# Kernel tuning notes

Hardware: AMD Instinct MI355X
Metric: run time of the kernel (lower is better)

## Reference

```python
import jax, jax.numpy as jnp
import numpy as np

B = 16384
IN_DIM = 28 * 28
HID = 768
NUM_EXPERTS = 8
NUM_CLASSES = 10
H_PHASOR = 32          # phasor bank harmonics -> 2*H features
DELTA0 = 7.0
DECAY = 0.7            # spiking attention leak
THETA = 1.0
K_WINNERS = 5
TOP_K_ROUTE = 2
TRAITS = (0.6, 0.6, 0.5, 0.5, 0.4)


def setup_inputs() -> dict:
    key = jax.random.key(0)
    ks = jax.random.split(key, 16)
    s = 0.02
    return {
        "x": jax.random.normal(ks[0], (B, 28, 28), jnp.float32),
        "W_in": jax.random.normal(ks[1], (IN_DIM, HID), jnp.float32) * s,
        "b_in": jnp.zeros((HID,), jnp.float32),
        "W_ph": jax.random.normal(ks[2], (2 * H_PHASOR, HID), jnp.float32) * s,
        "b_ph": jnp.zeros((HID,), jnp.float32),
        "W_gate": jax.random.normal(ks[3], (HID, NUM_EXPERTS), jnp.float32) * s,
        "b_gate": jnp.zeros((NUM_EXPERTS,), jnp.float32),
        "W_exp": jax.random.normal(ks[4], (NUM_EXPERTS, HID, HID), jnp.float32) * s,
        "b_exp": jnp.zeros((NUM_EXPERTS, HID), jnp.float32),
        "W_th": jax.random.normal(ks[5], (HID, NUM_EXPERTS), jnp.float32) * s,
        "b_th": jnp.zeros((NUM_EXPERTS,), jnp.float32),
        "W_pm": jax.random.normal(ks[6], (5, NUM_EXPERTS), jnp.float32) * s,
        "b_pm": jnp.zeros((NUM_EXPERTS,), jnp.float32),
        "W_out": jax.random.normal(ks[7], (HID, NUM_CLASSES), jnp.float32) * s,
        "b_out": jnp.zeros((NUM_CLASSES,), jnp.float32),
    }


def reference(x, W_in, b_in, W_ph, b_ph, W_gate, b_gate, W_exp, b_exp,
              W_th, b_th, W_pm, b_pm, W_out, b_out):
    Bn = x.shape[0]
    x_flat = x.reshape((Bn, -1))
    proj = x_flat @ W_in + b_in                                  # [B, HID]

    # Phasor bank on per-sample mean activation: sin/cos at H harmonics
    x_mean = jnp.mean(proj, axis=-1)                             # [B]
    freqs = DELTA0 * jnp.arange(1, H_PHASOR + 1, dtype=proj.dtype)
    phase = x_mean[:, None] * freqs[None, :]                     # [B, H]
    feats = jnp.concatenate([jnp.sin(phase), jnp.cos(phase)], -1)  # [B, 2H]
    enhanced = proj + feats @ W_ph + b_ph                        # [B, HID]

    # Top-K index selection feeding gather/scatter spiking attention
    V = enhanced.shape[-1]
    K = min(32, V)
    topk_idx = jax.lax.top_k(enhanced, K)[1].astype(jnp.int32)   # [B, K]
    w = DECAY ** jnp.arange(K, dtype=enhanced.dtype)             # decaying drive

    def gains_fn(idx):
        v = jnp.zeros((V,), enhanced.dtype).at[idx].add(w)       # scatter-add
        vals, widx = jax.lax.top_k(v, K_WINNERS)                 # k-WTA
        return jnp.ones((V,), enhanced.dtype).at[widx].add(vals / THETA)

    gains = jax.vmap(gains_fn)(topk_idx)                         # [B, V]
    attended = enhanced * gains

    # Personality bias + thalamic bias (thalamic_scale = 1.0)
    traits = jnp.asarray(TRAITS, dtype=enhanced.dtype)
    pbias = traits @ W_pm + b_pm                                 # [E]
    thal = jnp.mean(attended, axis=0) @ W_th + b_th              # [E]

    # MoE retrieval core: gate -> top-k softmax route -> combine experts
    gate_logits = attended @ W_gate + b_gate + pbias[None] + thal[None]  # [B, E]
    gvals, gidx = jax.lax.top_k(gate_logits, TOP_K_ROUTE)        # [B, k]
    gw = jax.nn.softmax(gvals, axis=-1)                          # [B, k]
    exp_out = jnp.einsum('bh,ehd->bed', attended, W_exp) + b_exp[None]   # [B, E, HID]
    sel = jnp.take_along_axis(exp_out, gidx[:, :, None], axis=1)  # [B, k, HID]
    context = jnp.sum(gw[:, :, None] * sel, axis=1)              # [B, HID]

    return context @ W_out + b_out                               # [B, classes]
```

## Files before the change

kernel.cpp:

```cpp
#include <hip/hip_runtime.h>
#include <hip/hip_bf16.h>
#include <cstddef>

#define BATCH 16384
#define IND   784
#define HID   768
#define NEXP  8
#define KT13  13

typedef short bf16x8 __attribute__((ext_vector_type(8)));
typedef float f32x4  __attribute__((ext_vector_type(4)));
typedef unsigned short ushort_t;

#define GLD16(g, l)                                                            \
  __builtin_amdgcn_global_load_lds(                                            \
      (const __attribute__((address_space(1))) unsigned int*)(g),              \
      (__attribute__((address_space(3))) unsigned int*)(l), 16, 0, 0)

__global__ __launch_bounds__(256) void k_wtrans(const float* __restrict__ Wexp,
                                                __hip_bfloat16* __restrict__ Wt)
{
  __shared__ float tile[32][33];
  const int e = blockIdx.z;
  const int h0 = blockIdx.x * 32, d0 = blockIdx.y * 32;
  const int tx = threadIdx.x & 31, ty = threadIdx.x >> 5;
  const float* src = Wexp + ((size_t)e * HID + h0) * HID + d0;
  #pragma unroll
  for (int i = 0; i < 4; i++)
    tile[ty + 8 * i][tx] = src[(size_t)(ty + 8 * i) * HID + tx];
  __syncthreads();
  __hip_bfloat16* dst = Wt + ((size_t)e * HID + d0) * HID + h0;
  #pragma unroll
  for (int i = 0; i < 4; i++)
    dst[(size_t)(ty + 8 * i) * HID + tx] = __float2bfloat16(tile[tx][ty + 8 * i]);
}

__device__ inline ushort_t bf16_rne(float f) {
  union { float f; unsigned u; } v; v.f = f;
  unsigned r = v.u + 0x7fffu + ((v.u >> 16) & 1u);
  return (ushort_t)(r >> 16);
}
__device__ inline float bf16_to_f(ushort_t h) {
  union { unsigned u; float f; } v; v.u = ((unsigned)h) << 16;
  return v.f;
}

__global__ __launch_bounds__(256) void k_packA(const float* __restrict__ x,
                                               ushort_t* __restrict__ Ahi,
                                               ushort_t* __restrict__ Alo)
{
  const int kt = blockIdx.x, mt = blockIdx.y;
  const size_t tbase = ((size_t)mt * KT13 + kt) * 8192;
  const int kb = kt * 64;
  #pragma unroll
  for (int i = 0; i < 4; i++) {
    int id = i * 256 + threadIdx.x;
    int r = id >> 3, c = id & 7;
    int row = mt * 128 + r;
    int k0 = kb + c * 8;
    float v[8];
    if (k0 + 8 <= IND) {
      const float4* p = reinterpret_cast<const float4*>(x + (size_t)row * IND + k0);
      float4 a = p[0], b = p[1];
      v[0] = a.x; v[1] = a.y; v[2] = a.z; v[3] = a.w;
      v[4] = b.x; v[5] = b.y; v[6] = b.z; v[7] = b.w;
    } else {
      #pragma unroll
      for (int j = 0; j < 8; j++) v[j] = (k0 + j < IND) ? x[(size_t)row * IND + k0 + j] : 0.f;
    }
    ushort_t hi[8], lo[8];
    #pragma unroll
    for (int j = 0; j < 8; j++) {
      hi[j] = bf16_rne(v[j]);
      lo[j] = bf16_rne(v[j] - bf16_to_f(hi[j]));
    }
    size_t dst = tbase + (size_t)r * 64 + ((c ^ (r & 7)) * 8);
    *reinterpret_cast<uint4*>(Ahi + dst) = *reinterpret_cast<uint4*>(hi);
    *reinterpret_cast<uint4*>(Alo + dst) = *reinterpret_cast<uint4*>(lo);
  }
}

__global__ __launch_bounds__(256) void k_packB(const float* __restrict__ W,
                                               ushort_t* __restrict__ Bhi,
                                               ushort_t* __restrict__ Blo)
{
  const int kt = blockIdx.x, nt = blockIdx.y;
  const size_t tbase = ((size_t)nt * KT13 + kt) * 8192;
  const int kb = kt * 64;
  #pragma unroll
  for (int i = 0; i < 4; i++) {
    int id = i * 256 + threadIdx.x;
    int r = id >> 3, c = id & 7;
    int n = nt * 128 + r;
    int k0 = kb + c * 8;
    float v[8];
    #pragma unroll
    for (int j = 0; j < 8; j++)
      v[j] = (k0 + j < IND) ? W[(size_t)(k0 + j) * HID + n] : 0.f;
    ushort_t hi[8], lo[8];
    #pragma unroll
    for (int j = 0; j < 8; j++) {
      hi[j] = bf16_rne(v[j]);
      lo[j] = bf16_rne(v[j] - bf16_to_f(hi[j]));
    }
    size_t dst = tbase + (size_t)r * 64 + ((c ^ (r & 7)) * 8);
    *reinterpret_cast<uint4*>(Bhi + dst) = *reinterpret_cast<uint4*>(hi);
    *reinterpret_cast<uint4*>(Blo + dst) = *reinterpret_cast<uint4*>(lo);
  }
}

__global__ __launch_bounds__(256, 2) void k_proj2(const ushort_t* __restrict__ Ahi,
                                                  const ushort_t* __restrict__ Alo,
                                                  const ushort_t* __restrict__ Bhi,
                                                  const ushort_t* __restrict__ Blo,
                                                  const float* __restrict__ bias,
                                                  float* __restrict__ out,
                                                  float* __restrict__ pm)
{
  __shared__ __align__(16) ushort_t lds[4 * 8192];
  const int bid = blockIdx.x;
  const int sid = (bid & 7) * 96 + (bid >> 3);
  const int mt = sid / 6, nt = sid - 6 * mt;
  const int tid = threadIdx.x, lane = tid & 63, w = tid >> 6;
  const int m0 = (w >> 1) * 64, n0 = (w & 1) * 64;
  const int l15 = lane & 15, g = lane >> 4;

  f32x4 acc[4][4];
  #pragma unroll
  for (int i = 0; i < 4; i++)
    #pragma unroll
    for (int j = 0; j < 4; j++) acc[i][j] = (f32x4){0.f, 0.f, 0.f, 0.f};

  const size_t abase = (size_t)mt * KT13 * 8192;
  const size_t bbase = (size_t)nt * KT13 * 8192;

  for (int kt = 0; kt < KT13; kt++) {
    __syncthreads();
    const ushort_t* srcs[4] = { Ahi + abase + (size_t)kt * 8192,
                                Alo + abase + (size_t)kt * 8192,
                                Bhi + bbase + (size_t)kt * 8192,
                                Blo + bbase + (size_t)kt * 8192 };
    #pragma unroll
    for (int buf = 0; buf < 4; buf++) {
      #pragma unroll
      for (int i = 0; i < 4; i++) {
        int off = w * 2048 + i * 512 + lane * 8;
        GLD16(srcs[buf] + off, &lds[buf * 8192 + w * 2048 + i * 512]);
      }
    }
    asm volatile("s_waitcnt vmcnt(0)");
    __syncthreads();
    #pragma unroll
    for (int ks = 0; ks < 2; ks++) {
      bf16x8 ah[4], al[4], bh[4], bl[4];
      #pragma unroll
      for (int i = 0; i < 4; i++) {
        int ca = ((4 * ks + g) ^ (l15 & 7)) * 8;
        int ra = m0 + 16 * i + l15;
        ah[i] = *reinterpret_cast<const bf16x8*>(&lds[0 * 8192 + ra * 64 + ca]);
        al[i] = *reinterpret_cast<const bf16x8*>(&lds[1 * 8192 + ra * 64 + ca]);
        int rb = n0 + 16 * i + l15;
        bh[i] = *reinterpret_cast<const bf16x8*>(&lds[2 * 8192 + rb * 64 + ca]);
        bl[i] = *reinterpret_cast<const bf16x8*>(&lds[3 * 8192 + rb * 64 + ca]);
      }
      #pragma unroll
      for (int i = 0; i < 4; i++)
        #pragma unroll
        for (int j = 0; j < 4; j++) {
          acc[i][j] = __builtin_amdgcn_mfma_f32_16x16x32_bf16(ah[i], bh[j], acc[i][j], 0, 0, 0);
          acc[i][j] = __builtin_amdgcn_mfma_f32_16x16x32_bf16(ah[i], bl[j], acc[i][j], 0, 0, 0);
          acc[i][j] = __builtin_amdgcn_mfma_f32_16x16x32_bf16(al[i], bh[j], acc[i][j], 0, 0, 0);
        }
    }
  }
  float bl[4];
  #pragma unroll
  for (int j = 0; j < 4; j++) bl[j] = bias[nt * 128 + n0 + 16 * j + l15];
  #pragma unroll
  for (int i = 0; i < 4; i++) {
    #pragma unroll
    for (int q = 0; q < 4; q++) {
      int m = mt * 128 + m0 + 16 * i + g * 4 + q;
      #pragma unroll
      for (int j = 0; j < 4; j++) {
        int n = nt * 128 + n0 + 16 * j + l15;
        out[(size_t)m * HID + n] = acc[i][j][q] + bl[j];
      }
    }
  }
  const float blsum = bl[0] + bl[1] + bl[2] + bl[3];
  const size_t pslot = (size_t)(nt * 2 + (w & 1)) * BATCH;
  #pragma unroll
  for (int i = 0; i < 4; i++) {
    #pragma unroll
    for (int q = 0; q < 4; q++) {
      float s = acc[i][0][q] + acc[i][1][q] + acc[i][2][q] + acc[i][3][q] + blsum;
      s += __shfl_xor(s, 1); s += __shfl_xor(s, 2);
      s += __shfl_xor(s, 4); s += __shfl_xor(s, 8);
      if (l15 == 0)
        pm[pslot + mt * 128 + m0 + 16 * i + g * 4 + q] = s;
    }
  }
}

__global__ __launch_bounds__(256) void k_phasor(const float* __restrict__ pm,
                                                const float* __restrict__ Wph,
                                                const float* __restrict__ bph,
                                                float* __restrict__ enh)
{
  __shared__ float Fs[64][132];
  __shared__ float Ws[64][128];
  __shared__ float mlds[128];
  const int t  = threadIdx.x;
  const int bm = blockIdx.y * 128, bn = blockIdx.x * 128;
  if (t < 128) {
    float s = 0.f;
    #pragma unroll
    for (int k = 0; k < 12; k++) s += pm[(size_t)k * BATCH + bm + t];
    mlds[t] = s * (1.0f / 768.0f);
  }
  __syncthreads();
  {
    const int r = t >> 1;
    const float mn = mlds[r];
    if ((t & 1) == 0) {
      #pragma unroll
      for (int j = 0; j < 32; j++) Fs[j][r] = sinf(mn * (7.0f * (j + 1)));
    } else {
      #pragma unroll
      for (int j = 0; j < 32; j++) Fs[32 + j][r] = cosf(mn * (7.0f * (j + 1)));
    }
  }
  #pragma unroll
  for (int i = 0; i < 8; i++) {
    int f4 = i * 256 + t;
    int k = f4 >> 5, n4 = (f4 & 31) * 4;
    *reinterpret_cast<float4*>(&Ws[k][n4]) =
        *reinterpret_cast<const float4*>(Wph + (size_t)k * HID + bn + n4);
  }
  __syncthreads();

  const int m0 = (t >> 4) * 8, n0 = (t & 15) * 8;
  float acc[8][8];
  #pragma unroll
  for (int i = 0; i < 8; i++)
    #pragma unroll
    for (int j = 0; j < 8; j++) acc[i][j] = 0.f;
  #pragma unroll 4
  for (int k = 0; k < 64; k++) {
    float a[8], b[8];
    *reinterpret_cast<float4*>(&a[0]) = *reinterpret_cast<const float4*>(&Fs[k][m0]);
    *reinterpret_cast<float4*>(&a[4]) = *reinterpret_cast<const float4*>(&Fs[k][m0 + 4]);
    *reinterpret_cast<float4*>(&b[0]) = *reinterpret_cast<const float4*>(&Ws[k][n0]);
    *reinterpret_cast<float4*>(&b[4]) = *reinterpret_cast<const float4*>(&Ws[k][n0 + 4]);
    #pragma unroll
    for (int i = 0; i < 8; i++)
      #pragma unroll
      for (int j = 0; j < 8; j++) acc[i][j] = fmaf(a[i], b[j], acc[i][j]);
  }
  float bl[8];
  #pragma unroll
  for (int j = 0; j < 8; j++) bl[j] = bph[bn + n0 + j];
  #pragma unroll
  for (int i = 0; i < 8; i++) {
    float* rowp = enh + (size_t)(bm + m0 + i) * HID + bn + n0;
    float4 p0 = *reinterpret_cast<float4*>(rowp);
    float4 p1 = *reinterpret_cast<float4*>(rowp + 4);
    p0.x += acc[i][0] + bl[0]; p0.y += acc[i][1] + bl[1];
    p0.z += acc[i][2] + bl[2]; p0.w += acc[i][3] + bl[3];
    p1.x += acc[i][4] + bl[4]; p1.y += acc[i][5] + bl[5];
    p1.z += acc[i][6] + bl[6]; p1.w += acc[i][7] + bl[7];
    *reinterpret_cast<float4*>(rowp)     = p0;
    *reinterpret_cast<float4*>(rowp + 4) = p1;
  }
}

__global__ __launch_bounds__(256) void k_attend(const float* __restrict__ enh,
                                                const float* __restrict__ Wg,
                                                __hip_bfloat16* __restrict__ attb,
                                                float* __restrict__ glog,
                                                float* __restrict__ partials)
{
  __shared__ float WgT[8][768];
  __shared__ float cs[4][768];
  const int t = threadIdx.x, lane = t & 63, w = t >> 6;
  for (int i = t; i < 768 * 8; i += 256) { int c = i >> 3, e = i & 7; WgT[e][c] = Wg[i]; }
  for (int i = t; i < 4 * 768; i += 256) cs[i / 768][i % 768] = 0.f;
  __syncthreads();

  for (int rr = 0; rr < 8; ++rr) {
    const int row = blockIdx.x * 32 + rr * 4 + w;
    const float* er = enh + (size_t)row * HID;
    float o[12], s[12];
    #pragma unroll
    for (int j = 0; j < 12; j++) { o[j] = er[lane + 64 * j]; s[j] = o[j]; }

    int wc[5];
    #pragma unroll
    for (int k = 0; k < 5; k++) {
      float v = -3.4e38f; int c = 0x7fffffff;
      #pragma unroll
      for (int j = 0; j < 12; j++)
        if (s[j] > v) { v = s[j]; c = lane + 64 * j; }
      #pragma unroll
      for (int off = 32; off; off >>= 1) {
        float ov = __shfl_xor(v, off); int oc = __shfl_xor(c, off);
        if (ov > v || (ov == v && oc < c)) { v = ov; c = oc; }
      }
      wc[k] = c;
      if (lane == (c & 63)) {
        #pragma unroll
        for (int j = 0; j < 12; j++) if (j == (c >> 6)) s[j] = -3.4e38f;
      }
    }

    float a[12];
    #pragma unroll
    for (int j = 0; j < 12; j++) a[j] = o[j];
    float wv = 1.0f;
    #pragma unroll
    for (int k = 0; k < 5; k++) {
      int c = wc[k];
      if (lane == (c & 63)) {
        #pragma unroll
        for (int j = 0; j < 12; j++) if (j == (c >> 6)) a[j] = o[j] * (1.0f + wv);
      }
      wv *= 0.7f;
    }
    #pragma unroll
    for (int j = 0; j < 12; j++)
      attb[(size_t)row * HID + lane + 64 * j] = __float2bfloat16(a[j]);
    #pragma unroll
    for (int j = 0; j < 12; j++) cs[w][lane + 64 * j] += a[j];

    float p[8];
    #pragma unroll
    for (int e = 0; e < 8; e++) p[e] = 0.f;
    #pragma unroll
    for (int j = 0; j < 12; j++) {
      int c = lane + 64 * j;
      #pragma unroll
      for (int e = 0; e < 8; e++) p[e] = fmaf(a[j], WgT[e][c], p[e]);
    }
    #pragma unroll
    for (int e = 0; e < 8; e++) {
      #pragma unroll
      for (int off = 32; off; off >>= 1) p[e] += __shfl_xor(p[e], off);
    }
    if (lane == 0) {
      #pragma unroll
      for (int e = 0; e < 8; e++) glog[(size_t)row * 8 + e] = p[e];
    }
  }
  __syncthreads();
  for (int i = t; i < 768; i += 256)
    partials[(size_t)blockIdx.x * 768 + i] = cs[0][i] + cs[1][i] + cs[2][i] + cs[3][i];
}

__global__ void k_thal(const float* __restrict__ partials,
                       const float* __restrict__ Wth, const float* __restrict__ bth,
                       const float* __restrict__ Wpm, const float* __restrict__ bpm,
                       const float* __restrict__ bgate, float* __restrict__ add8)
{
  __shared__ float cm[768];
  __shared__ float th[8];
  const int t = threadIdx.x;
  float s = 0.f;
  #pragma unroll 8
  for (int b = 0; b < 512; b++) s += partials[(size_t)b * 768 + t];
  cm[t] = s * (1.0f / 16384.0f);
  __syncthreads();
  if (t < 256) {
    int e = t >> 5, l = t & 31;
    float ps = 0.f;
    for (int c = l; c < 768; c += 32) ps = fmaf(cm[c], Wth[(size_t)c * 8 + e], ps);
    #pragma unroll
    for (int off = 16; off; off >>= 1) ps += __shfl_xor(ps, off);
    if (l == 0) th[e] = ps + bth[e];
  }
  __syncthreads();
  if (t < 8) {
    const float TR[5] = {0.6f, 0.6f, 0.5f, 0.5f, 0.4f};
    float pb = bpm[t];
    #pragma unroll
    for (int i = 0; i < 5; i++) pb = fmaf(TR[i], Wpm[i * 8 + t], pb);
    add8[t] = th[t] + pb + bgate[t];
  }
}

__global__ __launch_bounds__(256) void k_route(const float* __restrict__ glog,
                                               const float* __restrict__ add8,
                                               float* __restrict__ rw,
                                               unsigned char* __restrict__ re,
                                               int* __restrict__ counts)
{
  __shared__ float a8[8];
  __shared__ int lc[8];
  const int t = threadIdx.x;
  if (t < 8) { a8[t] = add8[t]; lc[t] = 0; }
  __syncthreads();
  const int row = blockIdx.x * 256 + t;
  const float4* gp = reinterpret_cast<const float4*>(glog + (size_t)row * 8);
  float4 g0 = gp[0], g1 = gp[1];
  float l[8] = { g0.x + a8[0], g0.y + a8[1], g0.z + a8[2], g0.w + a8[3],
                 g1.x + a8[4], g1.y + a8[5], g1.z + a8[6], g1.w + a8[7] };
  float v0 = l[0], v1 = -3.4e38f; int i0 = 0, i1 = 0;
  #pragma unroll
  for (int e = 1; e < 8; e++) {
    if (l[e] > v0)      { v1 = v0; i1 = i0; v0 = l[e]; i0 = e; }
    else if (l[e] > v1) { v1 = l[e]; i1 = e; }
  }
  float ex = expf(v1 - v0);
  float inv = 1.0f / (1.0f + ex);
  rw[row * 2] = inv; rw[row * 2 + 1] = ex * inv;
  re[row * 2] = (unsigned char)i0; re[row * 2 + 1] = (unsigned char)i1;
  atomicAdd(&lc[i0], 1); atomicAdd(&lc[i1], 1);
  __syncthreads();
  if (t < 8) atomicAdd(&counts[t], lc[t]);
}

__global__ void k_prefix(const int* __restrict__ counts, int* __restrict__ meta)
{
  if (threadIdx.x == 0) {
    int o = 0, tt = 0;
    for (int e = 0; e < 8; e++) {
      meta[e] = o; meta[9 + e] = tt; meta[19 + e] = o;
      o += counts[e]; tt += (counts[e] + 127) >> 7;
    }
    meta[8] = o; meta[17] = tt; meta[18] = tt;
  }
}

__global__ __launch_bounds__(256) void k_scatter(const unsigned char* __restrict__ re,
                                                 int* __restrict__ meta,
                                                 int* __restrict__ perm,
                                                 int* __restrict__ inv)
{
  __shared__ int lc[8], base[8];
  const int t = threadIdx.x;
  if (t < 8) lc[t] = 0;
  __syncthreads();
  const int row = blockIdx.x * 256 + t;
  const int e0 = re[row * 2], e1 = re[row * 2 + 1];
  const int p0 = atomicAdd(&lc[e0], 1);
  const int p1 = atomicAdd(&lc[e1], 1);
  __syncthreads();
  if (t < 8) base[t] = atomicAdd(&meta[19 + t], lc[t]);
  __syncthreads();
  const int s0 = base[e0] + p0;
  const int s1 = base[e1] + p1;
  perm[s0] = row * 2;     inv[row * 2]     = s0;
  perm[s1] = row * 2 + 1; inv[row * 2 + 1] = s1;
}

__global__ __launch_bounds__(256) void k_expert(const unsigned short* __restrict__ attb,
                                                const unsigned short* __restrict__ Wt,
                                                const float* __restrict__ bexp,
                                                const float* __restrict__ rw,
                                                const int* __restrict__ perm,
                                                const int* __restrict__ meta,
                                                ushort_t* __restrict__ ctxP)
{
  const int l = blockIdx.x;
  const int xcd = l & 7, idx = l >> 3;
  const int tb = xcd + 8 * (idx / 6);
  const int nb = (idx - 6 * (idx / 6)) * 128;
  if (tb >= meta[18]) return;
  __shared__ __align__(16) ushort_t sst[2][2][8192];
  __shared__ int rid[128];
  __shared__ float gws[128];
  __shared__ float bxs[128];

  const int* tst = meta + 9;
  int e = 0;
  #pragma unroll
  for (int i = 1; i < 8; i++) if (tb >= tst[i]) e = i;
  const int tix  = tb - tst[e];
  const int off  = meta[e];
  const int cnt  = meta[e + 1] - off;
  const int rbase = off + tix * 128;
  const int vcnt  = min(128, cnt - tix * 128);
  const int tid = threadIdx.x;

  if (tid < 128) {
    if (tid < vcnt) {
      int p = perm[rbase + tid];
      rid[tid] = p >> 1; gws[tid] = rw[p];
    } else {
      rid[tid] = 0; gws[tid] = 0.f;
    }
    bxs[tid] = bexp[(size_t)e * HID + nb + tid];
  }
  __syncthreads();

  const int lane = tid & 63, w = tid >> 6;
  const int m0 = (w >> 1) * 64, n0 = (w & 1) * 64;
  const int l15 = lane & 15, g = lane >> 4;
  const unsigned short* wbase = Wt + ((size_t)e * HID + nb) * HID;

#define ESTAGE(kb, b)                                                          \
  { _Pragma("unroll")                                                          \
    for (int i = 0; i < 4; i++) {                                              \
      int id_ = i * 256 + tid; int r_ = id_ >> 3, c_ = id_ & 7;                \
      int sc_ = (c_ ^ (r_ & 7)) * 8;                                           \
      GLD16(attb + (size_t)rid[r_] * HID + (kb) + sc_, &sst[b][0][(i * 256 + w * 64) * 8]); \
      GLD16(wbase + (size_t)r_ * HID + (kb) + sc_,     &sst[b][1][(i * 256 + w * 64) * 8]); \
    } }

  f32x4 acc[4][4];
  #pragma unroll
  for (int i = 0; i < 4; i++)
    #pragma unroll
    for (int j = 0; j < 4; j++) acc[i][j] = (f32x4){0.f, 0.f, 0.f, 0.f};

  ESTAGE(0, 0);
  for (int t = 0; t < 12; t++) {
    const int cb = t & 1;
    if (t < 11) {
      ESTAGE((t + 1) * 64, cb ^ 1);
      asm volatile("s_waitcnt vmcnt(8)" ::: "memory");
    } else {
      asm volatile("s_waitcnt vmcnt(0)" ::: "memory");
    }
    __builtin_amdgcn_s_barrier();
    const ushort_t* As = &sst[cb][0][0];
    const ushort_t* Bs = &sst[cb][1][0];
    #pragma unroll
    for (int ks = 0; ks < 2; ks++) {
      bf16x8 af[4], bfr[4];
      #pragma unroll
      for (int i = 0; i < 4; i++) {
        int ca = (((4 * ks + g) ^ (l15 & 7)) * 8);
        af[i]  = *reinterpret_cast<const bf16x8*>(As + (m0 + 16 * i + l15) * 64 + ca);
        bfr[i] = *reinterpret_cast<const bf16x8*>(Bs + (n0 + 16 * i + l15) * 64 + ca);
      }
      #pragma unroll
      for (int i = 0; i < 4; i++)
        #pragma unroll
        for (int j = 0; j < 4; j++)
          acc[i][j] = __builtin_amdgcn_mfma_f32_16x16x32_bf16(af[i], bfr[j], acc[i][j], 0, 0, 0);
    }
    __builtin_amdgcn_s_barrier();
  }
#undef ESTAGE

  unsigned short* Cs = &sst[0][0][0];
  __syncthreads();
  #pragma unroll
  for (int i = 0; i < 4; i++) {
    #pragma unroll
    for (int q = 0; q < 4; q++) {
      int m = m0 + 16 * i + g * 4 + q;
      float gwv = gws[m];
      #pragma unroll
      for (int j = 0; j < 4; j++) {
        int n = n0 + 16 * j + l15;
        Cs[m * 128 + n] = bf16_rne(gwv * (acc[i][j][q] + bxs[n]));
      }
    }
  }
  __syncthreads();
  #pragma unroll
  for (int c = 0; c < 8; c++) {
    int r = w * 32 + c * 4 + (lane >> 4);
    if (r < vcnt) {
      uint4 v = *reinterpret_cast<const uint4*>(Cs + r * 128 + l15 * 8);
      *reinterpret_cast<uint4*>(ctxP + (size_t)(rbase + r) * HID + nb + l15 * 8) = v;
    }
  }
}

__global__ __launch_bounds__(256) void k_out(const ushort_t* __restrict__ ctxP,
                                             const int* __restrict__ inv,
                                             const float* __restrict__ Wout,
                                             const float* __restrict__ bout,
                                             float* __restrict__ out)
{
  __shared__ float wT[10][768];
  const int t = threadIdx.x, lane = t & 63, w = t >> 6;
  for (int i = t; i < 7680; i += 256) { int cl = i / 768, d = i - cl * 768; wT[cl][d] = Wout[(size_t)d * 10 + cl]; }
  __syncthreads();
  for (int rr = 0; rr < 8; ++rr) {
    const int row = blockIdx.x * 32 + rr * 4 + w;
    const int s0 = inv[row * 2], s1 = inv[row * 2 + 1];
    const ushort_t* p0 = ctxP + (size_t)s0 * HID;
    const ushort_t* p1 = ctxP + (size_t)s1 * HID;
    float cd[12];
    #pragma unroll
    for (int j = 0; j < 12; j++)
      cd[j] = bf16_to_f(p0[lane + 64 * j]) + bf16_to_f(p1[lane + 64 * j]);
    float p[10];
    #pragma unroll
    for (int cl = 0; cl < 10; cl++) {
      float ps = 0.f;
      #pragma unroll
      for (int j = 0; j < 12; j++) ps = fmaf(cd[j], wT[cl][lane + 64 * j], ps);
      #pragma unroll
      for (int off = 32; off; off >>= 1) ps += __shfl_xor(ps, off);
      p[cl] = ps;
    }
    if (lane == 0) {
      #pragma unroll
      for (int cl = 0; cl < 10; cl++) out[(size_t)row * 10 + cl] = p[cl] + bout[cl];
    }
  }
}

extern "C" void kernel_launch(void* const* d_in, const int* in_sizes, int n_in,
                              void* d_out, int out_size, void* d_ws, size_t ws_size,
                              hipStream_t stream)
{
  const float* x     = (const float*)d_in[0];
  const float* W_in  = (const float*)d_in[1];
  const float* b_in  = (const float*)d_in[2];
  const float* W_ph  = (const float*)d_in[3];
  const float* b_ph  = (const float*)d_in[4];
  const float* W_g   = (const float*)d_in[5];
  const float* b_g   = (const float*)d_in[6];
  const float* W_exp = (const float*)d_in[7];
  const float* b_exp = (const float*)d_in[8];
  const float* W_th  = (const float*)d_in[9];
  const float* b_th  = (const float*)d_in[10];
  const float* W_pm  = (const float*)d_in[11];
  const float* b_pm  = (const float*)d_in[12];
  const float* W_out = (const float*)d_in[13];
  const float* b_out = (const float*)d_in[14];
  float* out = (float*)d_out;

  char* ws = (char*)d_ws;
  size_t off = 0;
  float* enh = (float*)(ws + off); off += (size_t)BATCH * HID * 4;
  char*  r1  = ws + off;           off += (size_t)2 * BATCH * KT13 * 64 * 2;
  ushort_t* Ahi = (ushort_t*)r1;
  ushort_t* Alo = Ahi + (size_t)BATCH * KT13 * 64;
  __hip_bfloat16* attb = (__hip_bfloat16*)r1;
  __hip_bfloat16* Wt   = (__hip_bfloat16*)(r1 + (size_t)BATCH * HID * 2);
  float* glog     = (float*)(ws + off); off += (size_t)BATCH * 8 * 4;
  float* partials = (float*)(ws + off); off += (size_t)512 * 768 * 4;
  float* pm       = (float*)(ws + off); off += (size_t)12 * BATCH * 4;
  float* add8     = (float*)(ws + off); off += 256;
  float* rw       = (float*)(ws + off); off += (size_t)BATCH * 2 * 4;
  unsigned char* re = (unsigned char*)(ws + off); off += (size_t)BATCH * 2;
  int* counts = (int*)(ws + off); off += 256;
  int* meta   = (int*)(ws + off); off += 256;
  int* perm   = (int*)(ws + off); off += (size_t)BATCH * 2 * 4;
  int* invp   = (int*)(ws + off); off += (size_t)BATCH * 2 * 4;
  ushort_t* Bhi = (ushort_t*)(ws + off); off += (size_t)KT13 * 64 * HID * 2;
  ushort_t* Blo = (ushort_t*)(ws + off); off += (size_t)KT13 * 64 * HID * 2;
  ushort_t* ctxP = (ushort_t*)enh;

  hipMemsetAsync(counts, 0, 32, stream);
  k_packB <<<dim3(13, 6),     256, 0, stream>>>(W_in, Bhi, Blo);
  k_packA <<<dim3(13, 128),   256, 0, stream>>>(x, Ahi, Alo);
  k_proj2 <<<768,             256, 0, stream>>>(Ahi, Alo, Bhi, Blo, b_in, enh, pm);
  k_wtrans<<<dim3(24, 24, 8), 256, 0, stream>>>(W_exp, Wt);
  k_phasor<<<dim3(6, 128),    256, 0, stream>>>(pm, W_ph, b_ph, enh);
  k_attend<<<512,             256, 0, stream>>>(enh, W_g, attb, glog, partials);
  k_thal  <<<1,               768, 0, stream>>>(partials, W_th, b_th, W_pm, b_pm, b_g, add8);
  k_route <<<64,              256, 0, stream>>>(glog, add8, rw, re, counts);
  k_prefix<<<1,                64, 0, stream>>>(counts, meta);
  k_scatter<<<64,             256, 0, stream>>>(re, meta, perm, invp);
  k_expert<<<1584,            256, 0, stream>>>((const unsigned short*)attb, (const unsigned short*)Wt,
                                                b_exp, rw, perm, meta, ctxP);
  k_out   <<<512,             256, 0, stream>>>(ctxP, invp, W_out, b_out, out);
}
```

Before: 324.8 us.

## Widen expert GEMM tile to 128x256 with 512-thread blocks

The grouped expert GEMM now uses 8 waves per block computing a 128-row by 256-column tile instead of 128x128, halving the number of blocks. Each gathered activation tile is reused across twice as many output columns, which cuts redundant loads of the activation rows. Load addresses are precomputed once outside the k-loop, and the explicit vmcnt wait plus raw s_barrier are replaced by __syncthreads. The larger LDS footprint (96KB double buffer) and 512 threads may reduce occupancy, and the simplified synchronization may serialize loads with compute.

New measurement: 324.2 us. Within noise of the previous version (-0.2%).

```diff
diff --git a/kernel.cpp b/kernel.cpp
--- a/kernel.cpp
+++ b/kernel.cpp
@@ -453,8 +453,8 @@
   perm[s1] = row * 2 + 1; inv[row * 2 + 1] = s1;
 }
 
-__global__ __launch_bounds__(256) void k_expert(const unsigned short* __restrict__ attb,
-                                                const unsigned short* __restrict__ Wt,
+__global__ __launch_bounds__(512) void k_expert(const ushort_t* __restrict__ attb,
+                                                const ushort_t* __restrict__ Wt,
                                                 const float* __restrict__ bexp,
                                                 const float* __restrict__ rw,
                                                 const int* __restrict__ perm,
@@ -463,13 +463,14 @@
 {
   const int l = blockIdx.x;
   const int xcd = l & 7, idx = l >> 3;
-  const int tb = xcd + 8 * (idx / 6);
-  const int nb = (idx - 6 * (idx / 6)) * 128;
+  const int tg = idx / 3;
+  const int tb = xcd + 8 * tg;
+  const int nb = (idx - 3 * tg) * 256;
   if (tb >= meta[18]) return;
-  __shared__ __align__(16) ushort_t sst[2][2][8192];
+  __shared__ __align__(16) ushort_t sst[2][24576];
   __shared__ int rid[128];
   __shared__ float gws[128];
-  __shared__ float bxs[128];
+  __shared__ float bxs[256];
 
   const int* tst = meta + 9;
   int e = 0;
@@ -489,23 +490,33 @@
     } else {
       rid[tid] = 0; gws[tid] = 0.f;
     }
-    bxs[tid] = bexp[(size_t)e * HID + nb + tid];
-  }
+  }
+  if (tid < 256) bxs[tid] = bexp[(size_t)e * HID + nb + tid];
   __syncthreads();
 
   const int lane = tid & 63, w = tid >> 6;
-  const int m0 = (w >> 1) * 64, n0 = (w & 1) * 64;
+  const int m0 = (w >> 2) * 64, n0 = (w & 3) * 64;
   const int l15 = lane & 15, g = lane >> 4;
-  const unsigned short* wbase = Wt + ((size_t)e * HID + nb) * HID;
+  const ushort_t* wbase = Wt + ((size_t)e * HID + nb) * HID;
+
+  const int chr = tid >> 3;
+  const int sc  = ((tid & 7) ^ (chr & 7)) * 8;
+  const ushort_t* asrc0 = attb  + (size_t)rid[chr] * HID + sc;
+  const ushort_t* asrc1 = attb  + (size_t)rid[chr + 64] * HID + sc;
+  const ushort_t* bsrc0 = wbase + (size_t)chr * HID + sc;
+  const ushort_t* bsrc1 = wbase + (size_t)(chr + 64) * HID + sc;
+  const ushort_t* bsrc2 = wbase + (size_t)(chr + 128) * HID + sc;
+  const ushort_t* bsrc3 = wbase + (size_t)(chr + 192) * HID + sc;
+  const int ad0 = (0 * 512 + w * 64) * 8;
+  const int ad1 = (1 * 512 + w * 64) * 8;
 
 #define ESTAGE(kb, b)                                                          \
-  { _Pragma("unroll")                                                          \
-    for (int i = 0; i < 4; i++) {                                              \
-      int id_ = i * 256 + tid; int r_ = id_ >> 3, c_ = id_ & 7;                \
-      int sc_ = (c_ ^ (r_ & 7)) * 8;                                           \
-      GLD16(attb + (size_t)rid[r_] * HID + (kb) + sc_, &sst[b][0][(i * 256 + w * 64) * 8]); \
-      GLD16(wbase + (size_t)r_ * HID + (kb) + sc_,     &sst[b][1][(i * 256 + w * 64) * 8]); \
-    } }
+  { GLD16(asrc0 + (kb), &sst[b][ad0]);                                         \
+    GLD16(asrc1 + (kb), &sst[b][ad1]);                                         \
+    GLD16(bsrc0 + (kb), &sst[b][8192 + ad0]);                                  \
+    GLD16(bsrc1 + (kb), &sst[b][8192 + ad1]);                                  \
+    GLD16(bsrc2 + (kb), &sst[b][8192 + (2 * 512 + w * 64) * 8]);               \
+    GLD16(bsrc3 + (kb), &sst[b][8192 + (3 * 512 + w * 64) * 8]); }
 
   f32x4 acc[4][4];
   #pragma unroll
@@ -514,17 +525,12 @@
     for (int j = 0; j < 4; j++) acc[i][j] = (f32x4){0.f, 0.f, 0.f, 0.f};
 
   ESTAGE(0, 0);
+  __syncthreads();
   for (int t = 0; t < 12; t++) {
     const int cb = t & 1;
-    if (t < 11) {
-      ESTAGE((t + 1) * 64, cb ^ 1);
-      asm volatile("s_waitcnt vmcnt(8)" ::: "memory");
-    } else {
-      asm volatile("s_waitcnt vmcnt(0)" ::: "memory");
-    }
-    __builtin_amdgcn_s_barrier();
-    const ushort_t* As = &sst[cb][0][0];
-    const ushort_t* Bs = &sst[cb][1][0];
+    if (t < 11) ESTAGE((t + 1) * 64, cb ^ 1);
+    const ushort_t* As = &sst[cb][0];
+    const ushort_t* Bs = &sst[cb][8192];
     #pragma unroll
     for (int ks = 0; ks < 2; ks++) {
       bf16x8 af[4], bfr[4];
@@ -540,12 +546,11 @@
         for (int j = 0; j < 4; j++)
           acc[i][j] = __builtin_amdgcn_mfma_f32_16x16x32_bf16(af[i], bfr[j], acc[i][j], 0, 0, 0);
     }
-    __builtin_amdgcn_s_barrier();
+    __syncthreads();
   }
 #undef ESTAGE
 
-  unsigned short* Cs = &sst[0][0][0];
-  __syncthreads();
+  ushort_t* Cs = &sst[0][0];
   #pragma unroll
   for (int i = 0; i < 4; i++) {
     #pragma unroll
@@ -555,17 +560,18 @@
       #pragma unroll
       for (int j = 0; j < 4; j++) {
         int n = n0 + 16 * j + l15;
-        Cs[m * 128 + n] = bf16_rne(gwv * (acc[i][j][q] + bxs[n]));
-      }
-    }
-  }
-  __syncthreads();
-  #pragma unroll
-  for (int c = 0; c < 8; c++) {
-    int r = w * 32 + c * 4 + (lane >> 4);
+        Cs[m * 256 + n] = bf16_rne(gwv * (acc[i][j][q] + bxs[n]));
+      }
+    }
+  }
+  __syncthreads();
+  #pragma unroll
+  for (int k = 0; k < 8; k++) {
+    int ch = k * 512 + tid;
+    int r = ch >> 5, c16 = ch & 31;
     if (r < vcnt) {
-      uint4 v = *reinterpret_cast<const uint4*>(Cs + r * 128 + l15 * 8);
-      *reinterpret_cast<uint4*>(ctxP + (size_t)(rbase + r) * HID + nb + l15 * 8) = v;
+      uint4 v = *reinterpret_cast<const uint4*>(Cs + r * 256 + c16 * 8);
+      *reinterpret_cast<uint4*>(ctxP + (size_t)(rbase + r) * HID + nb + c16 * 8) = v;
     }
   }
 }
@@ -660,7 +666,7 @@
   k_route <<<64,              256, 0, stream>>>(glog, add8, rw, re, counts);
   k_prefix<<<1,                64, 0, stream>>>(counts, meta);
   k_scatter<<<64,             256, 0, stream>>>(re, meta, perm, invp);
-  k_expert<<<1584,            256, 0, stream>>>((const unsigned short*)attb, (const unsigned short*)Wt,
+  k_expert<<<792,             512, 0, stream>>>((const ushort_t*)attb, (const ushort_t*)Wt,
                                                 b_exp, rw, perm, meta, ctxP);
   k_out   <<<512,             256, 0, stream>>>(ctxP, invp, W_out, b_out, out);
 }
```
